# Kernel tuning notes

Hardware: AMD Instinct MI355X
Metric: run time of the kernel (lower is better)

The kernel has to match this reference:

```python
import jax, jax.numpy as jnp
import numpy as np

DECAY = float(np.exp(-0.5))


def setup_inputs() -> dict:
    key = jax.random.key(0)
    k1, k2, k3, k4 = jax.random.split(key, 4)
    T, N, DR2 = 64, 2048, 512
    all_data_static = jax.random.normal(k1, (T, N, DR2), dtype=jnp.float32)
    threshold_nc = jax.random.uniform(k2, (T, N, 1), dtype=jnp.float32)
    all_data_dynamic_now = jax.random.uniform(k3, (N, DR2), dtype=jnp.float32)
    # RandomNormal(mean=1.0, stddev=0.5) initializer for w1 of shape (2*dr2, dr2)
    w1 = 1.0 + 0.5 * jax.random.normal(k4, (2 * DR2, DR2), dtype=jnp.float32)
    return {
        "all_data_static": all_data_static,
        "threshold_nc": threshold_nc,
        "all_data_dynamic_now": all_data_dynamic_now,
        "w1": w1,
    }


def reference(all_data_static, threshold_nc, all_data_dynamic_now, w1):
    # Gated recurrence per timestep:
    #   h <- sigmoid( (concat([h, static_t], -1) @ w1) * thr_t + h * (1 - thr_t) ) * exp(-1/2)
    # thr_t: [N, 1] broadcasts over dr2 (== tf.repeat along last axis).
    h0 = all_data_dynamic_now  # [N, dr2]

    def step(h, xs):
        static_t, thr_t = xs  # [N, dr2], [N, 1]
        mm = jnp.concatenate([h, static_t], axis=-1) @ w1  # [N, dr2]
        h_new = jax.nn.sigmoid(mm * thr_t + h * (1.0 - thr_t)) * DECAY
        return h_new, h_new

    _, states = jax.lax.scan(step, h0, (all_data_static, threshold_nc))  # [T, N, dr2]

    # Faithful to source: all_data_dynamic = [h0, states[1], ..., states[T-1]]
    # (the state after step 0 is used as carry but NOT stored).
    all_data_dynamic = jnp.concatenate([h0[None], states[1:]], axis=0)  # [T, N, dr2]
    all_data_dynamic_final = states[-1]  # [N, dr2]
    all_data_dynamic_diff = states[1:] - states[:-1]  # [T-1, N, dr2]
    return (all_data_dynamic, all_data_dynamic_final, all_data_dynamic_diff)
```

## Files before the change

### kernel.cpp

```cpp
#include <hip/hip_runtime.h>

#define NROWS 2048
#define DR2   512
#define TSTEPS 64
#define NK    ((size_t)NROWS * DR2)

typedef _Float16 half8 __attribute__((ext_vector_type(8)));
typedef float floatx4 __attribute__((ext_vector_type(4)));

static __device__ __forceinline__ void gload_lds16(const _Float16* g, _Float16* l) {
    __builtin_amdgcn_global_load_lds(
        (const __attribute__((address_space(1))) unsigned int*)g,
        (__attribute__((address_space(3))) unsigned int*)l,
        16, 0, 0);
}

__global__ void prep_w(const float* __restrict__ w1, _Float16* __restrict__ Wt) {
    int idx = blockIdx.x * 256 + threadIdx.x;
    int kk = idx & 1023;
    int j  = idx >> 10;
    Wt[idx] = (_Float16)w1[kk * DR2 + j];
}

__global__ void prep_h0(const float* __restrict__ h0, _Float16* __restrict__ h16,
                        float* __restrict__ out0) {
    int idx = blockIdx.x * 256 + threadIdx.x;
    float4 v = ((const float4*)h0)[idx];
    ((float4*)out0)[idx] = v;
    union { uint2 u; _Float16 h[4]; } p;
    p.h[0] = (_Float16)v.x; p.h[1] = (_Float16)v.y;
    p.h[2] = (_Float16)v.z; p.h[3] = (_Float16)v.w;
    ((uint2*)h16)[idx] = p.u;
}

#define KPP 128
__global__ __launch_bounds__(256) void precompute_S(
    const float* __restrict__ sta, const _Float16* __restrict__ Wt,
    float* S0, float* Srest)
{
    __shared__ _Float16 Ash[128 * KPP];
    __shared__ _Float16 Bsh[128 * KPP];
    const int tid = threadIdx.x, lane = tid & 63, wv = tid >> 6;
    const int waveM = wv & 1, waveJ = wv >> 1;
    const int lm = lane & 15, quad = lane >> 4;
    const int j0  = blockIdx.x * 128;
    const int mr0 = blockIdx.y * 128;
    const int t  = mr0 >> 11;
    const int n0 = mr0 & 2047;

    floatx4 acc[4][4] = {};

    for (int ph = 0; ph < 4; ++ph) {
        __syncthreads();
        #pragma unroll
        for (int i = 0; i < 8; ++i) {
            int rp = wv * 32 + i * 4;
            int r  = rp + (lane >> 4);
            int k8 = (lane & 15) ^ (r & 7);
            gload_lds16(Wt + (size_t)(j0 + r) * 1024 + 512 + ph * KPP + k8 * 8,
                        Bsh + rp * KPP);
        }
        #pragma unroll
        for (int p = 0; p < 8; ++p) {
            int c = p * 256 + tid;
            int r = c >> 4, c8p = c & 15;
            int k8 = c8p ^ (r & 7);
            size_t g = ((size_t)(mr0 + r)) * DR2 + ph * KPP + k8 * 8;
            float4 lo = *(const float4*)(sta + g);
            float4 hi = *(const float4*)(sta + g + 4);
            union { half8 v; _Float16 h[8]; } u;
            u.h[0]=(_Float16)lo.x; u.h[1]=(_Float16)lo.y;
            u.h[2]=(_Float16)lo.z; u.h[3]=(_Float16)lo.w;
            u.h[4]=(_Float16)hi.x; u.h[5]=(_Float16)hi.y;
            u.h[6]=(_Float16)hi.z; u.h[7]=(_Float16)hi.w;
            *(half8*)(Ash + r * KPP + (c8p << 3)) = u.v;
        }
        __syncthreads();

        #pragma unroll
        for (int ks = 0; ks < 4; ++ks) {
            int c8 = ks * 4 + quad;
            half8 a[4], b[4];
            #pragma unroll
            for (int tm = 0; tm < 4; ++tm) {
                int ra = waveM * 64 + tm * 16 + lm;
                a[tm] = *(const half8*)(Ash + ra * KPP + (((c8 ^ (ra & 7))) << 3));
            }
            #pragma unroll
            for (int tj = 0; tj < 4; ++tj) {
                int rb = waveJ * 64 + tj * 16 + lm;
                b[tj] = *(const half8*)(Bsh + rb * KPP + (((c8 ^ (rb & 7))) << 3));
            }
            #pragma unroll
            for (int tm = 0; tm < 4; ++tm)
                #pragma unroll
                for (int tj = 0; tj < 4; ++tj)
                    acc[tm][tj] = __builtin_amdgcn_mfma_f32_16x16x32_f16(
                        a[tm], b[tj], acc[tm][tj], 0, 0, 0);
        }
    }

    float* dst = (t == 0) ? S0 : (Srest + (size_t)(t - 1) * NK);
    #pragma unroll
    for (int tm = 0; tm < 4; ++tm) {
        #pragma unroll
        for (int r = 0; r < 4; ++r) {
            int n = n0 + waveM * 64 + tm * 16 + quad * 4 + r;
            #pragma unroll
            for (int tj = 0; tj < 4; ++tj) {
                int j = j0 + waveJ * 64 + tj * 16 + lm;
                dst[(size_t)n * DR2 + j] = acc[tm][tj][r];
            }
        }
    }
}

__global__ __launch_bounds__(256) void step_kernel(
    const float* __restrict__ thr,
    const _Float16* __restrict__ Wt,
    const _Float16* __restrict__ hprev,
    _Float16* __restrict__ hnext,
    const float* S,
    float* out0, float* __restrict__ out1, float* out2,
    int t)
{
    __shared__ _Float16 Ash[32 * 256];
    __shared__ _Float16 Bsh[64 * 256];
    const int tid = threadIdx.x, lane = tid & 63, wv = tid >> 6;
    const int waveM = wv & 1, waveJ = wv >> 1;
    const int lm = lane & 15, quad = lane >> 4;
    const int n0 = blockIdx.y * 32;
    const int j0 = blockIdx.x * 64;

    const int nb = n0 + waveM * 16 + quad * 4;
    const int jb = j0 + waveJ * 32 + lm;
    float thv[4], sv[2][4], hpv[2][4];
    #pragma unroll
    for (int r = 0; r < 4; ++r) {
        thv[r] = thr[t * NROWS + nb + r];
        #pragma unroll
        for (int tj = 0; tj < 2; ++tj) {
            size_t o = (size_t)(nb + r) * DR2 + jb + tj * 16;
            sv[tj][r]  = S[o];
            hpv[tj][r] = (float)hprev[o];
        }
    }

    floatx4 acc[2] = {};
    for (int ph = 0; ph < 2; ++ph) {
        __syncthreads();
        #pragma unroll
        for (int i = 0; i < 8; ++i) {
            int rp = wv * 16 + i * 2;
            int r  = rp + (lane >> 5);
            int k8 = (lane & 31) ^ (r & 7);
            gload_lds16(Wt + (size_t)(j0 + r) * 1024 + ph * 256 + k8 * 8,
                        Bsh + rp * 256);
        }
        #pragma unroll
        for (int i = 0; i < 4; ++i) {
            int rp = wv * 8 + i * 2;
            int r  = rp + (lane >> 5);
            int k8 = (lane & 31) ^ (r & 7);
            gload_lds16(hprev + (size_t)(n0 + r) * DR2 + ph * 256 + k8 * 8,
                        Ash + rp * 256);
        }
        __syncthreads();

        const int ra  = waveM * 16 + lm;
        const int rb0 = waveJ * 32 + lm, rb1 = rb0 + 16;
        #pragma unroll
        for (int ks = 0; ks < 8; ++ks) {
            int c8 = ks * 4 + quad;
            half8 a  = *(const half8*)(Ash + ra  * 256 + (((c8 ^ (ra  & 7))) << 3));
            half8 b0 = *(const half8*)(Bsh + rb0 * 256 + (((c8 ^ (rb0 & 7))) << 3));
            half8 b1 = *(const half8*)(Bsh + rb1 * 256 + (((c8 ^ (rb1 & 7))) << 3));
            acc[0] = __builtin_amdgcn_mfma_f32_16x16x32_f16(a, b0, acc[0], 0, 0, 0);
            acc[1] = __builtin_amdgcn_mfma_f32_16x16x32_f16(a, b1, acc[1], 0, 0, 0);
        }
    }

    const float DECAY = 0.60653065971263342f;
    #pragma unroll
    for (int r = 0; r < 4; ++r) {
        int n = nb + r;
        float om = 1.0f - thv[r];
        #pragma unroll
        for (int tj = 0; tj < 2; ++tj) {
            int j = jb + tj * 16;
            float z  = (acc[tj][r] + sv[tj][r]) * thv[r] + hpv[tj][r] * om;
            float hn = DECAY / (1.0f + __expf(-z));
            hnext[(size_t)n * DR2 + j] = (_Float16)hn;
            if (t >= 1) {
                size_t o = ((size_t)t * NROWS + n) * DR2 + j;
                out0[o] = hn;
                out2[o - NK] = hn - hpv[tj][r];
            }
            if (t == 63) out1[(size_t)n * DR2 + j] = hn;
        }
    }
}

extern "C" void kernel_launch(void* const* d_in, const int* in_sizes, int n_in,
                              void* d_out, int out_size, void* d_ws, size_t ws_size,
                              hipStream_t stream) {
    const float* d_static = (const float*)d_in[0];
    const float* d_thr    = (const float*)d_in[1];
    const float* d_h0     = (const float*)d_in[2];
    const float* d_w1     = (const float*)d_in[3];

    float* out0 = (float*)d_out;
    float* out1 = out0 + (size_t)TSTEPS * NK;
    float* out2 = out1 + NK;

    _Float16* Wt    = (_Float16*)d_ws;
    _Float16* hbuf0 = Wt + (size_t)DR2 * 1024;
    _Float16* hbuf1 = hbuf0 + NK;

    float* S0 = out0 + NK;

    prep_w<<<2048, 256, 0, stream>>>(d_w1, Wt);
    prep_h0<<<1024, 256, 0, stream>>>(d_h0, hbuf0, out0);
    precompute_S<<<dim3(4, 1024), 256, 0, stream>>>(d_static, Wt, S0, out2);

    dim3 grid(8, 64);
    for (int t = 0; t < TSTEPS; ++t) {
        const _Float16* hp = (t & 1) ? hbuf1 : hbuf0;
        _Float16*       hn = (t & 1) ? hbuf0 : hbuf1;
        const float*    S  = (t == 0) ? S0 : (out2 + (size_t)(t - 1) * NK);
        step_kernel<<<grid, 256, 0, stream>>>(d_thr, Wt, hp, hn, S,
                                              out0, out1, out2, t);
    }
}
```

Baseline: 1.293 ms.

## Fuse recurrence steps into one persistent kernel with LDS-resident hidden state

Replaces the 64 per-timestep launches with a single persistent kernel of 128 blocks. Each block owns 16 rows for all timesteps, keeps the fp16 hidden state double-buffered in LDS, and streams the recurrent half of W from global memory in a layout pre-arranged for MFMA fragments. The aim is to remove launch overhead and the global round-trips of the hidden state between steps. In exchange only 128 blocks occupy the GPU, and the W loads wait for completion before each MFMA chunk, so load latency is not overlapped with compute.

```diff
diff --git a/kernel.cpp b/kernel.cpp
--- a/kernel.cpp
+++ b/kernel.cpp
@@ -7,6 +7,8 @@
 
 typedef _Float16 half8 __attribute__((ext_vector_type(8)));
 typedef float floatx4 __attribute__((ext_vector_type(4)));
+
+#define WAITVM(N) __builtin_amdgcn_s_waitcnt(((N)&15) | (((N)>>4)<<14) | (7<<4) | (15<<8))
 
 static __device__ __forceinline__ void gload_lds16(const _Float16* g, _Float16* l) {
     __builtin_amdgcn_global_load_lds(
@@ -15,11 +17,24 @@
         16, 0, 0);
 }
 
-__global__ void prep_w(const float* __restrict__ w1, _Float16* __restrict__ Wt) {
+__global__ void prep_w(const float* __restrict__ w1, _Float16* __restrict__ Wq,
+                       _Float16* __restrict__ Wbot) {
     int idx = blockIdx.x * 256 + threadIdx.x;
-    int kk = idx & 1023;
-    int j  = idx >> 10;
-    Wt[idx] = (_Float16)w1[kk * DR2 + j];
+    if (idx < 262144) {
+        int e   = idx & 7;
+        int ln  = (idx >> 3) & 63;
+        int tl  = (idx >> 9) & 7;
+        int c   = (idx >> 12) & 15;
+        int J   = (idx >> 16) & 3;
+        int j   = J * 128 + tl * 16 + (ln & 15);
+        int k   = c * 32 + (ln >> 4) * 8 + e;
+        Wq[idx] = (_Float16)w1[k * DR2 + j];
+    } else {
+        int i  = idx - 262144;
+        int kk = i & 511;
+        int j  = i >> 9;
+        Wbot[i] = (_Float16)w1[(512 + kk) * DR2 + j];
+    }
 }
 
 __global__ void prep_h0(const float* __restrict__ h0, _Float16* __restrict__ h16,
@@ -35,7 +50,7 @@
 
 #define KPP 128
 __global__ __launch_bounds__(256) void precompute_S(
-    const float* __restrict__ sta, const _Float16* __restrict__ Wt,
+    const float* __restrict__ sta, const _Float16* __restrict__ Wbot,
     float* S0, float* Srest)
 {
     __shared__ _Float16 Ash[128 * KPP];
@@ -57,7 +72,7 @@
             int rp = wv * 32 + i * 4;
             int r  = rp + (lane >> 4);
             int k8 = (lane & 15) ^ (r & 7);
-            gload_lds16(Wt + (size_t)(j0 + r) * 1024 + 512 + ph * KPP + k8 * 8,
+            gload_lds16(Wbot + (size_t)(j0 + r) * 512 + ph * KPP + k8 * 8,
                         Bsh + rp * KPP);
         }
         #pragma unroll
@@ -102,7 +117,7 @@
 
     float* dst = (t == 0) ? S0 : (Srest + (size_t)(t - 1) * NK);
     #pragma unroll
-    for (int tm = 0; tm < 4; ++tm) {
+    for (int tm = 0; tm < 4; ++tm)
         #pragma unroll
         for (int r = 0; r < 4; ++r) {
             int n = n0 + waveM * 64 + tm * 16 + quad * 4 + r;
@@ -112,92 +127,92 @@
                 dst[(size_t)n * DR2 + j] = acc[tm][tj][r];
             }
         }
-    }
-}
-
-__global__ __launch_bounds__(256) void step_kernel(
+}
+
+__global__ __launch_bounds__(256, 1) void evolve(
     const float* __restrict__ thr,
-    const _Float16* __restrict__ Wt,
-    const _Float16* __restrict__ hprev,
-    _Float16* __restrict__ hnext,
-    const float* S,
-    float* out0, float* __restrict__ out1, float* out2,
-    int t)
+    const _Float16* __restrict__ Wq,
+    const _Float16* __restrict__ h16,
+    const float* S0,
+    float* out0, float* out1, float* out2)
 {
-    __shared__ _Float16 Ash[32 * 256];
-    __shared__ _Float16 Bsh[64 * 256];
-    const int tid = threadIdx.x, lane = tid & 63, wv = tid >> 6;
-    const int waveM = wv & 1, waveJ = wv >> 1;
-    const int lm = lane & 15, quad = lane >> 4;
-    const int n0 = blockIdx.y * 32;
-    const int j0 = blockIdx.x * 64;
-
-    const int nb = n0 + waveM * 16 + quad * 4;
-    const int jb = j0 + waveJ * 32 + lm;
-    float thv[4], sv[2][4], hpv[2][4];
+    __shared__ _Float16 hA[2][16 * 512];
+    __shared__ _Float16 Bst[4][4096];
+
+    const int tid  = threadIdx.x;
+    const int lane = tid & 63;
+    const int wv   = tid >> 6;
+    const int lm   = lane & 15;
+    const int quad = lane >> 4;
+    const int nb0  = blockIdx.x * 16;
+
     #pragma unroll
-    for (int r = 0; r < 4; ++r) {
-        thv[r] = thr[t * NROWS + nb + r];
-        #pragma unroll
-        for (int tj = 0; tj < 2; ++tj) {
-            size_t o = (size_t)(nb + r) * DR2 + jb + tj * 16;
-            sv[tj][r]  = S[o];
-            hpv[tj][r] = (float)hprev[o];
-        }
-    }
-
-    floatx4 acc[2] = {};
-    for (int ph = 0; ph < 2; ++ph) {
+    for (int i = 0; i < 4; ++i) {
+        int pos = tid + i * 256;
+        int r = pos >> 6, k8 = pos & 63;
+        uint4 v = *(const uint4*)(h16 + (size_t)(nb0 + r) * DR2 + k8 * 8);
+        *(uint4*)(&hA[0][r * 512 + ((k8 ^ (r & 7)) << 3)]) = v;
+    }
+    __syncthreads();
+
+    const _Float16* wq = Wq + (size_t)wv * 65536;
+    const float DECAY = 0.60653065971263342f;
+    int p = 0;
+
+    for (int t = 0; t < TSTEPS; ++t) {
+        const float* S_t = (t == 0) ? S0 : (out2 + (size_t)(t - 1) * NK);
+
+        half8 af[16];
+        #pragma unroll
+        for (int c = 0; c < 16; ++c)
+            af[c] = *(const half8*)(&hA[p][lm * 512 + (((c * 4 + quad) ^ (lm & 7)) << 3)]);
+
+        float thr_v = thr[t * NROWS + nb0 + lm];
+        float sv[8][4];
+        #pragma unroll
+        for (int tl = 0; tl < 8; ++tl)
+            #pragma unroll
+            for (int r = 0; r < 4; ++r)
+                sv[tl][r] = S_t[(size_t)(nb0 + quad * 4 + r) * DR2
+                                + wv * 128 + tl * 16 + lm];
+
+        floatx4 acc[8] = {};
+        for (int c = 0; c < 16; ++c) {
+            #pragma unroll
+            for (int g = 0; g < 8; ++g)
+                gload_lds16(wq + c * 4096 + g * 512 + lane * 8, Bst[wv] + g * 512);
+            WAITVM(0);
+            #pragma unroll
+            for (int tl = 0; tl < 8; ++tl) {
+                half8 b = *(const half8*)(&Bst[wv][tl * 512 + lane * 8]);
+                acc[tl] = __builtin_amdgcn_mfma_f32_16x16x32_f16(af[c], b, acc[tl], 0, 0, 0);
+            }
+        }
+
+        #pragma unroll
+        for (int r = 0; r < 4; ++r) {
+            int m = quad * 4 + r;
+            int n = nb0 + m;
+            float thv = __shfl(thr_v, m);
+            float om  = 1.0f - thv;
+            #pragma unroll
+            for (int tl = 0; tl < 8; ++tl) {
+                int jj = wv * 128 + tl * 16 + lm;
+                int sw = m * 512 + ((((jj >> 3) ^ (m & 7))) << 3) + (jj & 7);
+                float hp = (float)hA[p][sw];
+                float z  = (acc[tl][r] + sv[tl][r]) * thv + hp * om;
+                float hn = DECAY / (1.0f + __expf(-z));
+                hA[p ^ 1][sw] = (_Float16)hn;
+                if (t >= 1) {
+                    size_t o = ((size_t)t * NROWS + n) * DR2 + jj;
+                    out0[o] = hn;
+                    out2[o - NK] = hn - hp;
+                }
+                if (t == 63) out1[(size_t)n * DR2 + jj] = hn;
+            }
+        }
         __syncthreads();
-        #pragma unroll
-        for (int i = 0; i < 8; ++i) {
-            int rp = wv * 16 + i * 2;
-            int r  = rp + (lane >> 5);
-            int k8 = (lane & 31) ^ (r & 7);
-            gload_lds16(Wt + (size_t)(j0 + r) * 1024 + ph * 256 + k8 * 8,
-                        Bsh + rp * 256);
-        }
-        #pragma unroll
-        for (int i = 0; i < 4; ++i) {
-            int rp = wv * 8 + i * 2;
-            int r  = rp + (lane >> 5);
-            int k8 = (lane & 31) ^ (r & 7);
-            gload_lds16(hprev + (size_t)(n0 + r) * DR2 + ph * 256 + k8 * 8,
-                        Ash + rp * 256);
-        }
-        __syncthreads();
-
-        const int ra  = waveM * 16 + lm;
-        const int rb0 = waveJ * 32 + lm, rb1 = rb0 + 16;
-        #pragma unroll
-        for (int ks = 0; ks < 8; ++ks) {
-            int c8 = ks * 4 + quad;
-            half8 a  = *(const half8*)(Ash + ra  * 256 + (((c8 ^ (ra  & 7))) << 3));
-            half8 b0 = *(const half8*)(Bsh + rb0 * 256 + (((c8 ^ (rb0 & 7))) << 3));
-            half8 b1 = *(const half8*)(Bsh + rb1 * 256 + (((c8 ^ (rb1 & 7))) << 3));
-            acc[0] = __builtin_amdgcn_mfma_f32_16x16x32_f16(a, b0, acc[0], 0, 0, 0);
-            acc[1] = __builtin_amdgcn_mfma_f32_16x16x32_f16(a, b1, acc[1], 0, 0, 0);
-        }
-    }
-
-    const float DECAY = 0.60653065971263342f;
-    #pragma unroll
-    for (int r = 0; r < 4; ++r) {
-        int n = nb + r;
-        float om = 1.0f - thv[r];
-        #pragma unroll
-        for (int tj = 0; tj < 2; ++tj) {
-            int j = jb + tj * 16;
-            float z  = (acc[tj][r] + sv[tj][r]) * thv[r] + hpv[tj][r] * om;
-            float hn = DECAY / (1.0f + __expf(-z));
-            hnext[(size_t)n * DR2 + j] = (_Float16)hn;
-            if (t >= 1) {
-                size_t o = ((size_t)t * NROWS + n) * DR2 + j;
-                out0[o] = hn;
-                out2[o - NK] = hn - hpv[tj][r];
-            }
-            if (t == 63) out1[(size_t)n * DR2 + j] = hn;
-        }
+        p ^= 1;
     }
 }
 
@@ -213,22 +228,14 @@
     float* out1 = out0 + (size_t)TSTEPS * NK;
     float* out2 = out1 + NK;
 
-    _Float16* Wt    = (_Float16*)d_ws;
-    _Float16* hbuf0 = Wt + (size_t)DR2 * 1024;
-    _Float16* hbuf1 = hbuf0 + NK;
+    _Float16* Wq   = (_Float16*)d_ws;
+    _Float16* Wbot = Wq + 262144;
+    _Float16* h16  = Wbot + 262144;
 
     float* S0 = out0 + NK;
 
-    prep_w<<<2048, 256, 0, stream>>>(d_w1, Wt);
-    prep_h0<<<1024, 256, 0, stream>>>(d_h0, hbuf0, out0);
-    precompute_S<<<dim3(4, 1024), 256, 0, stream>>>(d_static, Wt, S0, out2);
-
-    dim3 grid(8, 64);
-    for (int t = 0; t < TSTEPS; ++t) {
-        const _Float16* hp = (t & 1) ? hbuf1 : hbuf0;
-        _Float16*       hn = (t & 1) ? hbuf0 : hbuf1;
-        const float*    S  = (t == 0) ? S0 : (out2 + (size_t)(t - 1) * NK);
-        step_kernel<<<grid, 256, 0, stream>>>(d_thr, Wt, hp, hn, S,
-                                              out0, out1, out2, t);
-    }
-}
+    prep_w<<<2048, 256, 0, stream>>>(d_w1, Wq, Wbot);
+    prep_h0<<<1024, 256, 0, stream>>>(d_h0, h16, out0);
+    precompute_S<<<dim3(4, 1024), 256, 0, stream>>>(d_static, Wbot, S0, out2);
+    evolve<<<128, 256, 0, stream>>>(d_thr, Wq, h16, S0, out0, out1, out2);
+}
```

Result: slower. 1.504 ms (+16.3%).
